# Kernel tuning notes

Measured on AMD Instinct MI355X. Metric: run time of the kernel, lower is better.

## Reference

```python
import jax, jax.numpy as jnp
import numpy as np

# SLAYER neuron / simulation hyperparameters (from network.yaml)
THETA = 10.0      # spike threshold
TAU_SR = 10.0     # SRM (PSP) kernel time constant [ms]
TAU_REF = 1.0     # refractory kernel time constant [ms]
SCALE_REF = 2.0   # refractory kernel scale
TS = 1.0          # simulation step [ms]
K_SRM = 100       # truncation length of SRM kernel (eps decays ~0 by 10*tau)
K_REF = 32        # truncation length of refractory kernel (tauRef=1 -> decays fast)


def _eps_kernel(tau, k):
    # eps(t) = (t/tau) * exp(1 - t/tau), eps(0) = 0  (SLAYER SRM alpha kernel)
    t = jnp.arange(k, dtype=jnp.float32) * TS
    return (t / tau) * jnp.exp(1.0 - t / tau)


def psp(x, kern):
    # Causal temporal filter: y[..., t] = sum_j kern[j] * x[..., t - j]
    B, N, T = x.shape
    lhs = x.reshape(B * N, 1, T)
    rhs = kern[::-1].reshape(1, 1, -1)  # lax.conv is cross-correlation -> flip
    y = jax.lax.conv_general_dilated(
        lhs, rhs, window_strides=(1,), padding=[(kern.shape[0] - 1, 0)],
        dimension_numbers=('NCH', 'OIH', 'NCH'))
    return y.reshape(B, N, T)


def spike(u, refk):
    # Sequential thresholding with refractory feedback (SLAYER spikeFunction fwd).
    # u: [B, N, T] membrane drive. State r: future refractory contributions.
    kr = refk.shape[0]
    refk_shift = jnp.concatenate([refk[1:], jnp.zeros((1,), refk.dtype)])

    def step(r, u_t):
        m = u_t + r[..., 0]                      # membrane potential at t
        s = (m >= THETA).astype(u_t.dtype)       # hard spike
        r_next = jnp.concatenate([r[..., 1:], jnp.zeros_like(r[..., :1])], -1) \
                 + s[..., None] * refk_shift     # add refractory response
        return r_next, s

    uT = jnp.moveaxis(u, -1, 0)                  # [T, B, N]
    r0 = jnp.zeros(uT.shape[1:] + (kr,), u.dtype)
    _, sT = jax.lax.scan(step, r0, uT)
    return jnp.moveaxis(sT, 0, -1) / TS          # [B, N, T]


def setup_inputs() -> dict:
    key = jax.random.key(0)
    k1, k2, k3 = jax.random.split(key, 3)
    B, NIN, NHID, NOUT, T = 32, 2048, 512, 10, 350
    spike_input = (jax.random.uniform(k1, (B, NIN, T)) < 0.05).astype(jnp.float32)
    W1 = jax.random.normal(k2, (NHID, NIN), dtype=jnp.float32) * 0.05
    W2 = jax.random.normal(k3, (NOUT, NHID), dtype=jnp.float32) * 0.05
    return {"spike_input": spike_input, "W1": W1, "W2": W2}


def reference(spike_input, W1, W2):
    srm = _eps_kernel(TAU_SR, K_SRM)
    refk = -SCALE_REF * THETA * _eps_kernel(TAU_REF, K_REF)
    # layer 1: psp -> dense -> spike
    a1 = jnp.einsum('bnt,mn->bmt', psp(spike_input, srm), W1)
    s1 = spike(a1, refk)
    # layer 2: psp -> dense -> spike
    a2 = jnp.einsum('bnt,mn->bmt', psp(s1, srm), W2)
    s2 = spike(a2, refk)
    return s2
```

## Files before the change

### kernel.cpp

```cpp
#include <hip/hip_runtime.h>
#include <stdint.h>

static constexpr int B  = 32;
static constexpr int T  = 350;
static constexpr int NIN = 2048;
static constexpr int NH  = 512;
static constexpr int NO  = 10;
static constexpr int BT  = B * T;

static constexpr float THETA = 10.0f;
static constexpr float BETA  = 0.36787944117144233f;
static constexpr float CREF  = 54.365636569180904707f;

static constexpr size_t OFF_W1TS = 0;
static constexpr size_t OFF_MASK = 4196352;
static constexpr size_t OFF_SRM  = 7080960;
static constexpr size_t OFF_Z1   = 7081984;
static constexpr size_t OFF_A1   = 30019584;
static constexpr size_t OFF_LST  = OFF_A1;
static constexpr size_t OFF_CNT  = OFF_A1 + 4300800;
static constexpr size_t OFF_SMK  = 52957184;

static constexpr int SLICE_F = 8;
static constexpr int NSLICE  = NH / SLICE_F;
static constexpr int SLICE_STRIDE = 2049 * SLICE_F;

__global__ void __launch_bounds__(256) k_prep(const float* __restrict__ x,
                                              const float* __restrict__ W1,
                                              float* __restrict__ W1Ts,
                                              uint64_t* __restrict__ mask,
                                              float* __restrict__ srm28) {
    int bid = blockIdx.x;
    if (bid < 1024) {
        __shared__ uint64_t tb[6][64];
        int b = bid >> 5, nblk = bid & 31;
        int wv = threadIdx.x >> 6, lane = threadIdx.x & 63;
        for (int g = 0; g < 4; ++g) {
            float v[4][6];
            #pragma unroll
            for (int i = 0; i < 4; ++i) {
                int nr = wv + 4 * (4 * g + i);
                const float* xp = x + ((size_t)b * NIN + nblk * 64 + nr) * T;
                #pragma unroll
                for (int c = 0; c < 6; ++c) {
                    int t = c * 64 + lane;
                    v[i][c] = (t < T) ? xp[t] : 0.f;
                }
            }
            #pragma unroll
            for (int i = 0; i < 4; ++i) {
                int nr = wv + 4 * (4 * g + i);
                #pragma unroll
                for (int c = 0; c < 6; ++c) {
                    uint64_t mk = __ballot(v[i][c] != 0.0f);
                    if (lane == 0) tb[c][nr] = mk;
                }
            }
        }
        __syncthreads();
        static const uint64_t AM[6] = {
            0x00000000FFFFFFFFull, 0x0000FFFF0000FFFFull, 0x00FF00FF00FF00FFull,
            0x0F0F0F0F0F0F0F0Full, 0x3333333333333333ull, 0x5555555555555555ull };
        for (int c = wv; c < 6; c += 4) {
            uint64_t w = tb[c][lane];
            #pragma unroll
            for (int i = 0; i < 6; ++i) {
                int s = 32 >> i;
                uint64_t A = AM[i];
                uint64_t y = __shfl_xor((unsigned long long)w, s);
                if ((lane & s) == 0) w = (w & A)  | ((y & A) << s);
                else                 w = (w & ~A) | ((y & ~A) >> s);
            }
            int t = c * 64 + lane;
            if (t < T) mask[((size_t)b * 32 + nblk) * 352 + t] = w;
        }
    } else if (bid < 2048) {
        __shared__ float tile[32][33];
        int idx = bid - 1024;
        int n0 = (idx & 63) * 32, m0 = (idx >> 6) * 32;
        int tx = threadIdx.x & 31, ty0 = threadIdx.x >> 5;
        #pragma unroll
        for (int i = 0; i < 4; ++i) {
            int ty = ty0 + 8 * i;
            tile[ty][tx] = W1[(size_t)(m0 + ty) * NIN + n0 + tx];
        }
        __syncthreads();
        #pragma unroll
        for (int i = 0; i < 4; ++i) {
            int ty = ty0 + 8 * i;
            int n = n0 + ty, m = m0 + tx;
            W1Ts[(size_t)(m >> 3) * SLICE_STRIDE + n * SLICE_F + (m & 7)] = tile[tx][ty];
        }
    } else {
        int j = threadIdx.x;
        if (j < 192) {
            float v = 0.f;
            int i = j - 28;
            if (i >= 0 && i < 100) { float t = (float)i; v = (t * 0.1f) * expf(1.f - t * 0.1f); }
            srm28[j] = v;
        }
        for (int i = j; i < NSLICE * SLICE_F; i += 256)
            W1Ts[(size_t)(i >> 3) * SLICE_STRIDE + 2048 * SLICE_F + (i & 7)] = 0.f;
    }
}

__global__ void __launch_bounds__(64) k_decode(const uint64_t* __restrict__ mask,
                                               uint16_t* __restrict__ glst,
                                               int* __restrict__ gcnt) {
    __shared__ uint16_t lst[192];
    int t = blockIdx.x, b = blockIdx.y;
    int row = b * T + t;
    int lane = threadIdx.x;
    uint64_t w = (lane < 32) ? mask[((size_t)b * 32 + lane) * 352 + t] : 0ull;
    int cnt = __popcll(w);
    int pre = cnt;
    #pragma unroll
    for (int off = 1; off < 64; off <<= 1) {
        int v = __shfl_up(pre, off);
        if (lane >= off) pre += v;
    }
    int total = __shfl(pre, 63);
    int excl = pre - cnt;
    while (w) {
        int bit = __builtin_ctzll(w);
        w &= w - 1;
        lst[excl++] = (uint16_t)((lane << 6) + bit);
    }
    int padded = (total + 7) & ~7;
    if (lane < padded - total) lst[total + lane] = 2048;
    __syncthreads();
    uint16_t* op = glst + (size_t)row * 192;
    for (int i = lane; i < padded; i += 64) op[i] = lst[i];
    if (lane == 0) gcnt[row] = padded;
}

__global__ void __launch_bounds__(256) k_z1s(const uint16_t* __restrict__ glst,
                                             const int* __restrict__ gcnt,
                                             const float* __restrict__ W1Ts,
                                             float* __restrict__ z1) {
    __shared__ float w1s[SLICE_STRIDE];
    int s = blockIdx.x;
    int bt0 = blockIdx.y * (BT / 8);
    const float4* src = (const float4*)(W1Ts + (size_t)s * SLICE_STRIDE);
    for (int i = threadIdx.x; i < SLICE_STRIDE / 4; i += 256)
        ((float4*)w1s)[i] = src[i];
    __syncthreads();

    int q  = threadIdx.x & 1;
    int rl = threadIdx.x >> 1;
    for (int rr = rl; rr < BT / 8; rr += 128) {
        int row = bt0 + rr;
        int padded = gcnt[row];
        const ushort4* lp = (const ushort4*)(glst + (size_t)row * 192);
        float4 acc = {0, 0, 0, 0};
        for (int k = 0; k < padded; k += 8) {
            ushort4 q0 = lp[k >> 2];
            ushort4 q1 = lp[(k >> 2) + 1];
            const float* base = w1s + q * 4;
            float4 x0 = *(const float4*)(base + q0.x * SLICE_F);
            float4 x1 = *(const float4*)(base + q0.y * SLICE_F);
            float4 x2 = *(const float4*)(base + q0.z * SLICE_F);
            float4 x3 = *(const float4*)(base + q0.w * SLICE_F);
            float4 x4 = *(const float4*)(base + q1.x * SLICE_F);
            float4 x5 = *(const float4*)(base + q1.y * SLICE_F);
            float4 x6 = *(const float4*)(base + q1.z * SLICE_F);
            float4 x7 = *(const float4*)(base + q1.w * SLICE_F);
            acc.x += x0.x; acc.y += x0.y; acc.z += x0.z; acc.w += x0.w;
            acc.x += x1.x; acc.y += x1.y; acc.z += x1.z; acc.w += x1.w;
            acc.x += x2.x; acc.y += x2.y; acc.z += x2.z; acc.w += x2.w;
            acc.x += x3.x; acc.y += x3.y; acc.z += x3.z; acc.w += x3.w;
            acc.x += x4.x; acc.y += x4.y; acc.z += x4.z; acc.w += x4.w;
            acc.x += x5.x; acc.y += x5.y; acc.z += x5.z; acc.w += x5.w;
            acc.x += x6.x; acc.y += x6.y; acc.z += x6.z; acc.w += x6.w;
            acc.x += x7.x; acc.y += x7.y; acc.z += x7.z; acc.w += x7.w;
        }
        *(float4*)(z1 + (size_t)row * NH + s * SLICE_F + q * 4) = acc;
    }
}

__global__ void __launch_bounds__(64) k_fir1(const float* __restrict__ src,
                                             float* __restrict__ dst,
                                             const float* __restrict__ srm28) {
    __shared__ float tb[192];
    int b = blockIdx.x, half = blockIdx.y, tg = blockIdx.z;
    int lane = threadIdx.x;
    for (int i = lane; i < 192; i += 64) tb[i] = srm28[i];
    __syncthreads();
    int t0 = tg * 16;
    int m = half * 256 + lane * 4;
    const float* sp = src + (size_t)b * T * NH + m;

    float4 acc[16];
    #pragma unroll
    for (int r = 0; r < 16; ++r) acc[r] = make_float4(0.f, 0.f, 0.f, 0.f);
    float c[16];
    #pragma unroll
    for (int r = 0; r < 16; ++r) c[r] = tb[r + 127];

    for (int o = 0; o < 8; ++o) {
        #pragma unroll
        for (int j = 0; j < 16; ++j) {
            int dd = o * 16 + j;
            int tau = t0 - 99 + dd;
            float4 v = make_float4(0.f, 0.f, 0.f, 0.f);
            if (tau >= 0 && tau < T) v = *(const float4*)(sp + (size_t)tau * NH);
            #pragma unroll
            for (int r = 0; r < 16; ++r) {
                acc[r].x += c[r] * v.x; acc[r].y += c[r] * v.y;
                acc[r].z += c[r] * v.z; acc[r].w += c[r] * v.w;
            }
            #pragma unroll
            for (int r = 15; r > 0; --r) c[r] = c[r - 1];
            int ci = 126 - dd;
            c[0] = tb[ci < 0 ? 0 : ci];
        }
    }
    #pragma unroll
    for (int r = 0; r < 16; ++r) {
        int t = t0 + r;
        if (t < T) *(float4*)(dst + ((size_t)b * T + t) * NH + m) = acc[r];
    }
}

__global__ void __launch_bounds__(64) k_scan1(const float* __restrict__ a1,
                                              uint64_t* __restrict__ smaskg) {
    constexpr int CT = 16;
    constexpr int NC = (T + CT - 1) / CT;
    int tid = blockIdx.x * 64 + threadIdx.x;
    int b = tid >> 9, m = tid & 511;
    int w8 = m >> 6;
    const float* up = a1 + (size_t)b * T * NH + m;
    float A = 0.f, Bs = 0.f;
    float c0[CT], c1[CT], c2[CT];
    #pragma unroll
    for (int j = 0; j < CT; ++j) c0[j] = up[(size_t)j * NH];
    #pragma unroll
    for (int j = 0; j < CT; ++j) {
        int t = CT + j;
        c1[j] = (t < T) ? up[(size_t)t * NH] : 0.f;
    }
    for (int c = 0; c < NC; ++c) {
        int t0 = c * CT;
        int nsteps = (T - t0 < CT) ? (T - t0) : CT;
        if (c + 2 < NC) {
            #pragma unroll
            for (int j = 0; j < CT; ++j) {
                int t = t0 + 2 * CT + j;
                c2[j] = (t < T) ? up[(size_t)t * NH] : 0.f;
            }
        }
        #pragma unroll
        for (int j = 0; j < CT; ++j) {
            if (j < nsteps) {
                float mem = c0[j] - CREF * Bs;
                float sp = (mem >= THETA) ? 1.0f : 0.0f;
                A = sp + BETA * A;
                Bs = BETA * (Bs + A);
                uint64_t mk = __ballot(sp != 0.0f);
                if (threadIdx.x == 0) smaskg[((size_t)b * T + t0 + j) * 8 + w8] = mk;
            }
        }
        #pragma unroll
        for (int j = 0; j < CT; ++j) { c0[j] = c1[j]; c1[j] = c2[j]; }
    }
}

__global__ void __launch_bounds__(256) k_tail(const uint64_t* __restrict__ smaskg,
                                              const float* __restrict__ W2,
                                              const float* __restrict__ srm28,
                                              float* __restrict__ out) {
    __shared__ float w2s_ab[NO * NH];
    __shared__ uint64_t smk[T * 8];
    __shared__ float tb[192];
    __shared__ float zb[350 * 11 + 16];
    int b = blockIdx.x, tid = threadIdx.x;
    for (int i = tid; i < NO * NH; i += 256) w2s_ab[i] = W2[i];
    const uint64_t* mp = smaskg + (size_t)b * T * 8;
    for (int i = tid; i < T * 8; i += 256) smk[i] = mp[i];
    if (tid < 192) tb[tid] = srm28[tid];
    __syncthreads();
    for (int i = tid; i < T * NO; i += 256) {
        int t = i / NO, o = i - t * NO;
        const float* wrow = w2s_ab + o * NH;
        float acc = 0.f;
        #pragma unroll
        for (int w8 = 0; w8 < 8; ++w8) {
            uint64_t mk = smk[t * 8 + w8];
            int base = w8 * 64;
            while (mk) {
                int bit = __builtin_ctzll(mk);
                mk &= mk - 1;
                acc += wrow[base + bit];
            }
        }
        zb[t * 11 + o] = acc;
    }
    __syncthreads();
    float* ab = w2s_ab;
    if (tid < 220) {
        int tt = tid / 10, o = tid - tt * 10;
        int t0 = tt * 16;
        float acc[16];
        #pragma unroll
        for (int r = 0; r < 16; ++r) acc[r] = 0.f;
        float c[16];
        #pragma unroll
        for (int r = 0; r < 16; ++r) c[r] = tb[r + 127];
        for (int oo = 0; oo < 8; ++oo) {
            #pragma unroll
            for (int j = 0; j < 16; ++j) {
                int dd = oo * 16 + j;
                int tau = t0 - 99 + dd;
                float v = (tau >= 0 && tau < T) ? zb[tau * 11 + o] : 0.f;
                #pragma unroll
                for (int r = 0; r < 16; ++r) acc[r] += c[r] * v;
                #pragma unroll
                for (int r = 15; r > 0; --r) c[r] = c[r - 1];
                int ci = 126 - dd;
                c[0] = tb[ci < 0 ? 0 : ci];
            }
        }
        #pragma unroll
        for (int r = 0; r < 16; ++r) {
            int t = t0 + r;
            if (t < T) ab[t * 10 + o] = acc[r];
        }
    }
    __syncthreads();
    if (tid < NO) {
        int o = tid;
        float A2 = 0.f, B2 = 0.f;
        float* op = out + ((size_t)b * NO + o) * T;
        for (int t = 0; t < T; ++t) {
            float mem = ab[t * 10 + o] - CREF * B2;
            float sp = (mem >= THETA) ? 1.0f : 0.0f;
            A2 = sp + BETA * A2;
            B2 = BETA * (B2 + A2);
            op[t] = sp;
        }
    }
}

extern "C" void kernel_launch(void* const* d_in, const int* in_sizes, int n_in,
                              void* d_out, int out_size, void* d_ws, size_t ws_size,
                              hipStream_t stream) {
    const float* x  = (const float*)d_in[0];
    const float* W1 = (const float*)d_in[1];
    const float* W2 = (const float*)d_in[2];
    char* ws = (char*)d_ws;
    float*    W1Ts   = (float*)(ws + OFF_W1TS);
    uint64_t* mask   = (uint64_t*)(ws + OFF_MASK);
    float*    srm    = (float*)(ws + OFF_SRM);
    float*    z1     = (float*)(ws + OFF_Z1);
    float*    a1     = (float*)(ws + OFF_A1);
    uint16_t* glst   = (uint16_t*)(ws + OFF_LST);
    int*      gcnt   = (int*)(ws + OFF_CNT);
    uint64_t* smaskg = (uint64_t*)(ws + OFF_SMK);
    float*    out    = (float*)d_out;

    hipLaunchKernelGGL(k_prep,   dim3(2049),      dim3(256), 0, stream, x, W1, W1Ts, mask, srm);
    hipLaunchKernelGGL(k_decode, dim3(T, B),      dim3(64),  0, stream, mask, glst, gcnt);
    hipLaunchKernelGGL(k_z1s,    dim3(NSLICE, 8), dim3(256), 0, stream, glst, gcnt, W1Ts, z1);
    hipLaunchKernelGGL(k_fir1,   dim3(B, 2, 22),  dim3(64),  0, stream, z1, a1, srm);
    hipLaunchKernelGGL(k_scan1,  dim3(256),       dim3(64),  0, stream, a1, smaskg);
    hipLaunchKernelGGL(k_tail,   dim3(B),         dim3(256), 0, stream, smaskg, W2, srm, out);
}
```

Before: 298.0 us.

## Split sparse gather GEMM into LDS-slice blocks and L2-gather row blocks

```diff
diff --git a/kernel.cpp b/kernel.cpp
--- a/kernel.cpp
+++ b/kernel.cpp
@@ -12,22 +12,29 @@
 static constexpr float BETA  = 0.36787944117144233f;
 static constexpr float CREF  = 54.365636569180904707f;
 
-static constexpr size_t OFF_W1TS = 0;
-static constexpr size_t OFF_MASK = 4196352;
-static constexpr size_t OFF_SRM  = 7080960;
-static constexpr size_t OFF_Z1   = 7081984;
-static constexpr size_t OFF_A1   = 30019584;
-static constexpr size_t OFF_LST  = OFF_A1;
-static constexpr size_t OFF_CNT  = OFF_A1 + 4300800;
-static constexpr size_t OFF_SMK  = 52957184;
-
 static constexpr int SLICE_F = 8;
 static constexpr int NSLICE  = NH / SLICE_F;
 static constexpr int SLICE_STRIDE = 2049 * SLICE_F;
 
+static constexpr int NCHUNK  = 5;
+static constexpr int CHROWS  = 1280;
+static constexpr int RL      = NCHUNK * CHROWS;
+static constexpr int NL2BLK  = (BT - RL) / 4;
+
+static constexpr size_t OFF_W1TS = 0;
+static constexpr size_t OFF_W1T  = 4196352;
+static constexpr size_t OFF_MASK = 8392704;
+static constexpr size_t OFF_SRM  = 11276288;
+static constexpr size_t OFF_Z1   = 11277312;
+static constexpr size_t OFF_A1   = 34214912;
+static constexpr size_t OFF_LST  = OFF_A1;
+static constexpr size_t OFF_CNT  = OFF_A1 + 4300800;
+static constexpr size_t OFF_SMK  = 57152512;
+
 __global__ void __launch_bounds__(256) k_prep(const float* __restrict__ x,
                                               const float* __restrict__ W1,
                                               float* __restrict__ W1Ts,
+                                              float* __restrict__ W1T,
                                               uint64_t* __restrict__ mask,
                                               float* __restrict__ srm28) {
     int bid = blockIdx.x;
@@ -89,7 +96,9 @@
         for (int i = 0; i < 4; ++i) {
             int ty = ty0 + 8 * i;
             int n = n0 + ty, m = m0 + tx;
-            W1Ts[(size_t)(m >> 3) * SLICE_STRIDE + n * SLICE_F + (m & 7)] = tile[tx][ty];
+            float v = tile[tx][ty];
+            W1Ts[(size_t)(m >> 3) * SLICE_STRIDE + n * SLICE_F + (m & 7)] = v;
+            W1T[(size_t)n * NH + m] = v;
         }
     } else {
         int j = threadIdx.x;
@@ -101,6 +110,8 @@
         }
         for (int i = j; i < NSLICE * SLICE_F; i += 256)
             W1Ts[(size_t)(i >> 3) * SLICE_STRIDE + 2048 * SLICE_F + (i & 7)] = 0.f;
+        for (int i = j; i < NH; i += 256)
+            W1T[(size_t)2048 * NH + i] = 0.f;
     }
 }
 
@@ -134,47 +145,96 @@
     if (lane == 0) gcnt[row] = padded;
 }
 
-__global__ void __launch_bounds__(256) k_z1s(const uint16_t* __restrict__ glst,
+__global__ void __launch_bounds__(256) k_z1h(const uint16_t* __restrict__ glst,
                                              const int* __restrict__ gcnt,
                                              const float* __restrict__ W1Ts,
+                                             const float* __restrict__ W1T,
                                              float* __restrict__ z1) {
     __shared__ float w1s[SLICE_STRIDE];
-    int s = blockIdx.x;
-    int bt0 = blockIdx.y * (BT / 8);
-    const float4* src = (const float4*)(W1Ts + (size_t)s * SLICE_STRIDE);
-    for (int i = threadIdx.x; i < SLICE_STRIDE / 4; i += 256)
-        ((float4*)w1s)[i] = src[i];
-    __syncthreads();
-
-    int q  = threadIdx.x & 1;
-    int rl = threadIdx.x >> 1;
-    for (int rr = rl; rr < BT / 8; rr += 128) {
-        int row = bt0 + rr;
+    int bid = blockIdx.x;
+    if (bid < NSLICE * NCHUNK) {
+        int s = bid % NSLICE;
+        int bt0 = (bid / NSLICE) * CHROWS;
+        const float4* src = (const float4*)(W1Ts + (size_t)s * SLICE_STRIDE);
+        for (int i = threadIdx.x; i < SLICE_STRIDE / 4; i += 256)
+            ((float4*)w1s)[i] = src[i];
+        __syncthreads();
+        int q  = threadIdx.x & 1;
+        int rl = threadIdx.x >> 1;
+        for (int rr = rl; rr < CHROWS; rr += 128) {
+            int row = bt0 + rr;
+            int padded = gcnt[row];
+            const ushort4* lp = (const ushort4*)(glst + (size_t)row * 192);
+            float4 acc = {0, 0, 0, 0};
+            for (int k = 0; k < padded; k += 8) {
+                ushort4 q0 = lp[k >> 2];
+                ushort4 q1 = lp[(k >> 2) + 1];
+                const float* base = w1s + q * 4;
+                float4 x0 = *(const float4*)(base + q0.x * SLICE_F);
+                float4 x1 = *(const float4*)(base + q0.y * SLICE_F);
+                float4 x2 = *(const float4*)(base + q0.z * SLICE_F);
+                float4 x3 = *(const float4*)(base + q0.w * SLICE_F);
+                float4 x4 = *(const float4*)(base + q1.x * SLICE_F);
+                float4 x5 = *(const float4*)(base + q1.y * SLICE_F);
+                float4 x6 = *(const float4*)(base + q1.z * SLICE_F);
+                float4 x7 = *(const float4*)(base + q1.w * SLICE_F);
+                acc.x += x0.x; acc.y += x0.y; acc.z += x0.z; acc.w += x0.w;
+                acc.x += x1.x; acc.y += x1.y; acc.z += x1.z; acc.w += x1.w;
+                acc.x += x2.x; acc.y += x2.y; acc.z += x2.z; acc.w += x2.w;
+                acc.x += x3.x; acc.y += x3.y; acc.z += x3.z; acc.w += x3.w;
+                acc.x += x4.x; acc.y += x4.y; acc.z += x4.z; acc.w += x4.w;
+                acc.x += x5.x; acc.y += x5.y; acc.z += x5.z; acc.w += x5.w;
+                acc.x += x6.x; acc.y += x6.y; acc.z += x6.z; acc.w += x6.w;
+                acc.x += x7.x; acc.y += x7.y; acc.z += x7.z; acc.w += x7.w;
+            }
+            *(float4*)(z1 + (size_t)row * NH + s * SLICE_F + q * 4) = acc;
+        }
+    } else {
+        int wv = threadIdx.x >> 6, lane = threadIdx.x & 63;
+        int row = RL + (bid - NSLICE * NCHUNK) * 4 + wv;
         int padded = gcnt[row];
         const ushort4* lp = (const ushort4*)(glst + (size_t)row * 192);
-        float4 acc = {0, 0, 0, 0};
+        const float4* W4 = (const float4*)W1T;
+        float4 a0 = {0,0,0,0}, a1v = {0,0,0,0};
+        int i0 = lane * 2, i1 = lane * 2 + 1;
         for (int k = 0; k < padded; k += 8) {
             ushort4 q0 = lp[k >> 2];
             ushort4 q1 = lp[(k >> 2) + 1];
-            const float* base = w1s + q * 4;
-            float4 x0 = *(const float4*)(base + q0.x * SLICE_F);
-            float4 x1 = *(const float4*)(base + q0.y * SLICE_F);
-            float4 x2 = *(const float4*)(base + q0.z * SLICE_F);
-            float4 x3 = *(const float4*)(base + q0.w * SLICE_F);
-            float4 x4 = *(const float4*)(base + q1.x * SLICE_F);
-            float4 x5 = *(const float4*)(base + q1.y * SLICE_F);
-            float4 x6 = *(const float4*)(base + q1.z * SLICE_F);
-            float4 x7 = *(const float4*)(base + q1.w * SLICE_F);
-            acc.x += x0.x; acc.y += x0.y; acc.z += x0.z; acc.w += x0.w;
-            acc.x += x1.x; acc.y += x1.y; acc.z += x1.z; acc.w += x1.w;
-            acc.x += x2.x; acc.y += x2.y; acc.z += x2.z; acc.w += x2.w;
-            acc.x += x3.x; acc.y += x3.y; acc.z += x3.z; acc.w += x3.w;
-            acc.x += x4.x; acc.y += x4.y; acc.z += x4.z; acc.w += x4.w;
-            acc.x += x5.x; acc.y += x5.y; acc.z += x5.z; acc.w += x5.w;
-            acc.x += x6.x; acc.y += x6.y; acc.z += x6.z; acc.w += x6.w;
-            acc.x += x7.x; acc.y += x7.y; acc.z += x7.z; acc.w += x7.w;
-        }
-        *(float4*)(z1 + (size_t)row * NH + s * SLICE_F + q * 4) = acc;
+            const float4* p0 = W4 + (size_t)q0.x * 128;
+            const float4* p1 = W4 + (size_t)q0.y * 128;
+            const float4* p2 = W4 + (size_t)q0.z * 128;
+            const float4* p3 = W4 + (size_t)q0.w * 128;
+            const float4* p4 = W4 + (size_t)q1.x * 128;
+            const float4* p5 = W4 + (size_t)q1.y * 128;
+            const float4* p6 = W4 + (size_t)q1.z * 128;
+            const float4* p7 = W4 + (size_t)q1.w * 128;
+            float4 x0 = p0[i0], y0 = p0[i1];
+            float4 x1 = p1[i0], y1 = p1[i1];
+            float4 x2 = p2[i0], y2 = p2[i1];
+            float4 x3 = p3[i0], y3 = p3[i1];
+            float4 x4 = p4[i0], y4 = p4[i1];
+            float4 x5 = p5[i0], y5 = p5[i1];
+            float4 x6 = p6[i0], y6 = p6[i1];
+            float4 x7 = p7[i0], y7 = p7[i1];
+            a0.x += x0.x; a0.y += x0.y; a0.z += x0.z; a0.w += x0.w;
+            a1v.x += y0.x; a1v.y += y0.y; a1v.z += y0.z; a1v.w += y0.w;
+            a0.x += x1.x; a0.y += x1.y; a0.z += x1.z; a0.w += x1.w;
+            a1v.x += y1.x; a1v.y += y1.y; a1v.z += y1.z; a1v.w += y1.w;
+            a0.x += x2.x; a0.y += x2.y; a0.z += x2.z; a0.w += x2.w;
+            a1v.x += y2.x; a1v.y += y2.y; a1v.z += y2.z; a1v.w += y2.w;
+            a0.x += x3.x; a0.y += x3.y; a0.z += x3.z; a0.w += x3.w;
+            a1v.x += y3.x; a1v.y += y3.y; a1v.z += y3.z; a1v.w += y3.w;
+            a0.x += x4.x; a0.y += x4.y; a0.z += x4.z; a0.w += x4.w;
+            a1v.x += y4.x; a1v.y += y4.y; a1v.z += y4.z; a1v.w += y4.w;
+            a0.x += x5.x; a0.y += x5.y; a0.z += x5.z; a0.w += x5.w;
+            a1v.x += y5.x; a1v.y += y5.y; a1v.z += y5.z; a1v.w += y5.w;
+            a0.x += x6.x; a0.y += x6.y; a0.z += x6.z; a0.w += x6.w;
+            a1v.x += y6.x; a1v.y += y6.y; a1v.z += y6.z; a1v.w += y6.w;
+            a0.x += x7.x; a0.y += x7.y; a0.z += x7.z; a0.w += x7.w;
+            a1v.x += y7.x; a1v.y += y7.y; a1v.z += y7.z; a1v.w += y7.w;
+        }
+        float4* zp = (float4*)(z1 + (size_t)row * NH);
+        zp[i0] = a0; zp[i1] = a1v;
     }
 }
 
@@ -349,6 +409,7 @@
     const float* W2 = (const float*)d_in[2];
     char* ws = (char*)d_ws;
     float*    W1Ts   = (float*)(ws + OFF_W1TS);
+    float*    W1T    = (float*)(ws + OFF_W1T);
     uint64_t* mask   = (uint64_t*)(ws + OFF_MASK);
     float*    srm    = (float*)(ws + OFF_SRM);
     float*    z1     = (float*)(ws + OFF_Z1);
@@ -358,10 +419,10 @@
     uint64_t* smaskg = (uint64_t*)(ws + OFF_SMK);
     float*    out    = (float*)d_out;
 
-    hipLaunchKernelGGL(k_prep,   dim3(2049),      dim3(256), 0, stream, x, W1, W1Ts, mask, srm);
-    hipLaunchKernelGGL(k_decode, dim3(T, B),      dim3(64),  0, stream, mask, glst, gcnt);
-    hipLaunchKernelGGL(k_z1s,    dim3(NSLICE, 8), dim3(256), 0, stream, glst, gcnt, W1Ts, z1);
-    hipLaunchKernelGGL(k_fir1,   dim3(B, 2, 22),  dim3(64),  0, stream, z1, a1, srm);
-    hipLaunchKernelGGL(k_scan1,  dim3(256),       dim3(64),  0, stream, a1, smaskg);
-    hipLaunchKernelGGL(k_tail,   dim3(B),         dim3(256), 0, stream, smaskg, W2, srm, out);
-}
+    hipLaunchKernelGGL(k_prep,   dim3(2049),                       dim3(256), 0, stream, x, W1, W1Ts, W1T, mask, srm);
+    hipLaunchKernelGGL(k_decode, dim3(T, B),                       dim3(64),  0, stream, mask, glst, gcnt);
+    hipLaunchKernelGGL(k_z1h,    dim3(NSLICE * NCHUNK + NL2BLK),   dim3(256), 0, stream, glst, gcnt, W1Ts, W1T, z1);
+    hipLaunchKernelGGL(k_fir1,   dim3(B, 2, 22),                   dim3(64),  0, stream, z1, a1, srm);
+    hipLaunchKernelGGL(k_scan1,  dim3(256),                        dim3(64),  0, stream, a1, smaskg);
+    hipLaunchKernelGGL(k_tail,   dim3(B),                          dim3(256), 0, stream, smaskg, W2, srm, out);
+}
```

New measurement: 321.5 us. 7.9% more time.
